# Kernel optimization log

Measured on AMD Instinct MI355X. Metric: run time of the kernel, lower is better.

## Reference

```python
import jax, jax.numpy as jnp
import numpy as np
from jax import lax

MAX_DIST_THR = 10.0
R = 10  # window radius: any distance < thr has per-axis offset <= 9, so R=10 is exact after clamping
INF = jnp.float32(1e12)


def _min_pass(c, axis):
    # 1D min-convolution with squared offsets: out[i] = min_k (c[i+k-R] + (k-R)^2)
    n = c.shape[axis]
    pad = [(0, 0)] * c.ndim
    pad[axis] = (R, R)
    p = jnp.pad(c, pad, constant_values=INF)
    out = None
    for k in range(2 * R + 1):
        v = lax.slice_in_dim(p, k, k + n, axis=axis) + jnp.float32((k - R) ** 2)
        out = v if out is None else jnp.minimum(out, v)
    return out


def _clamped_edt(fg):
    # Euclidean distance to nearest True pixel, exact where < MAX_DIST_THR, clamped above.
    cost = jnp.where(fg, jnp.float32(0.0), INF)  # [B,1,H,W]
    d2 = _min_pass(_min_pass(cost, 2), 3)
    return jnp.minimum(jnp.sqrt(d2), jnp.float32(MAX_DIST_THR))


def reference(gt, pred):
    thr = jnp.float32(MAX_DIST_THR)
    D_gt = lax.stop_gradient(_clamped_edt(gt > 0.5))
    D_est = lax.stop_gradient(_clamped_edt(pred > 0.5))
    mask_D_gt = D_gt < thr
    filt_sum = jnp.sum(pred * mask_D_gt)
    # ch[ch > thr] = thr  ==  minimum (values are non-negative)
    ch1 = jnp.minimum(D_gt * pred, thr)
    ch2 = jnp.minimum(D_est * gt, thr)
    num = jnp.sum(ch1 + ch2, axis=(1, 2, 3))  # [B]
    den = jnp.mean(jnp.sum(pred, axis=(1, 2, 3)) + jnp.sum(gt, axis=(1, 2, 3)))  # scalar
    dbe_com = num / den
    return jnp.where(filt_sum == 0, thr, dbe_com)


def setup_inputs() -> dict:
    key = jax.random.key(0)
    k1, k2 = jax.random.split(key)
    shape = (1, 1, 2048, 4096)
    gt = jax.random.bernoulli(k1, 0.05, shape).astype(jnp.float32)
    pred = jax.random.bernoulli(k2, 0.05, shape).astype(jnp.float32)
    return {"gt": gt, "pred": pred}
```

## Files before the change

kernel.cpp:

```cpp
#include <hip/hip_runtime.h>

typedef unsigned long long u64;
typedef unsigned int u32;

#define HH 2048
#define WW 4096
#define MW 66
#define MROWS (HH + 20)
#define MASK_WORDS ((size_t)MROWS * MW)
#define MASK_BYTES (MASK_WORDS * 8)
#define THR 10.0f
#define LIST_CAP (512u * 1024u)

#define PACK_BLOCKS 2048
#define COMP_BLOCKS 256
#define SCAN_BLOCKS 1024
#define GUARD_WORDS 5416

#define GM_OFF 16384
#define PM_OFF (GM_OFF + MASK_BYTES)
#define LP_OFF (PM_OFF + MASK_BYTES)
#define LG_OFF (LP_OFF + LIST_CAP * 4)

__global__ __launch_bounds__(256) void pack_masks(const float* __restrict__ gt,
                                                  const float* __restrict__ pred,
                                                  u64* __restrict__ gm,
                                                  u64* __restrict__ pm,
                                                  u32* __restrict__ cnt) {
    int gtid = blockIdx.x * 256 + threadIdx.x;
    if (gtid < 2) cnt[gtid] = 0u;
    if (gtid < 2 * GUARD_WORDS) {
        int m = gtid >= GUARD_WORDS;
        int i = gtid - m * GUARD_WORDS;
        u64* dst = m ? pm : gm;
        int row, w;
        if (i < 660)       { row = i / 66;            w = i - row * 66; }
        else if (i < 1320) { int j = i - 660; int r = j / 66;
                             row = (MROWS - 10) + r;  w = j - r * 66; }
        else               { int j = i - 1320; row = 10 + (j >> 1);
                             w = (j & 1) ? (MW - 1) : 0; }
        dst[(size_t)row * MW + w] = 0ull;
    }

    int l = threadIdx.x & 63;
    int gw = gtid >> 6;
    #pragma unroll 1
    for (int t = 0; t < 4; ++t) {
        int tile = gw * 4 + t;
        int base = tile * 256;
        u64 g0 = __ballot(gt[base +   0 + l] > 0.5f);
        u64 g1 = __ballot(gt[base +  64 + l] > 0.5f);
        u64 g2 = __ballot(gt[base + 128 + l] > 0.5f);
        u64 g3 = __ballot(gt[base + 192 + l] > 0.5f);
        u64 p0 = __ballot(pred[base +   0 + l] > 0.5f);
        u64 p1 = __ballot(pred[base +  64 + l] > 0.5f);
        u64 p2 = __ballot(pred[base + 128 + l] > 0.5f);
        u64 p3 = __ballot(pred[base + 192 + l] > 0.5f);
        if (l < 4) {
            u64 gv = (l == 0) ? g0 : (l == 1) ? g1 : (l == 2) ? g2 : g3;
            u64 pv = (l == 0) ? p0 : (l == 1) ? p1 : (l == 2) ? p2 : p3;
            int W = tile * 4 + l;
            size_t o = (size_t)((W >> 6) + 10) * MW + 1 + (W & 63);
            gm[o] = gv;
            pm[o] = pv;
        }
    }
}

__global__ __launch_bounds__(256) void compact(const u64* __restrict__ gm,
                                               const u64* __restrict__ pm,
                                               u32* __restrict__ cnt,
                                               u32* __restrict__ listP,
                                               u32* __restrict__ listG) {
    bool isPred = blockIdx.x < (COMP_BLOCKS / 2);
    const u64* msk = isPred ? pm : gm;
    u32* lst = isPred ? listP : listG;
    u32* ctr = isPred ? cnt : cnt + 1;
    int wb = (blockIdx.x & (COMP_BLOCKS / 2 - 1)) * 1024;
    int tid = threadIdx.x;

    u64 wv[4];
    u32 tp = 0;
    #pragma unroll
    for (int j = 0; j < 4; ++j) {
        int W = wb + tid + 256 * j;
        wv[j] = msk[(size_t)((W >> 6) + 10) * MW + 1 + (W & 63)];
        tp += (u32)__popcll(wv[j]);
    }
    u32 s = tp;
    #pragma unroll
    for (int o = 1; o < 64; o <<= 1) {
        u32 v = __shfl_up(s, o);
        if ((tid & 63) >= o) s += v;
    }
    u32 excl = s - tp;
    __shared__ u32 wtot[4], wbase[4], sbase;
    int wid = tid >> 6, lane = tid & 63;
    if (lane == 63) wtot[wid] = s;
    __syncthreads();
    if (tid == 0) {
        u32 bt = 0;
        for (int i = 0; i < 4; ++i) { wbase[i] = bt; bt += wtot[i]; }
        sbase = atomicAdd(ctr, bt);
    }
    __syncthreads();
    u32 ptr = sbase + wbase[wid] + excl;
    #pragma unroll
    for (int j = 0; j < 4; ++j) {
        int W = wb + tid + 256 * j;
        u32 yx = ((u32)(W >> 6) << 12) | ((u32)(W & 63) << 6);
        u64 m = wv[j];
        while (m) {
            u32 b = (u32)__ffsll((long long)m) - 1u;
            if (ptr < LIST_CAP) lst[ptr] = yx + b;
            ++ptr;
            m &= m - 1;
        }
    }
}

__device__ __forceinline__ u32 scan_d2(const u64* __restrict__ rowc, int x) {
    int b = x + 54;
    int sh = b & 63;
    int shl = 63 - sh;
    const u64* q = rowc + (b >> 6);
    u64 q0 = q[0], q1 = q[1];
    u32 win = (u32)((q0 >> sh) | ((q1 << 1) << shl)) & 0x1FFFFFu;
    u32 hi = win >> 10;
    u32 lo = win & 0x3FFu;
    u32 dr = (u32)__ffs((int)hi) - 1u;
    u32 dl = (u32)__clz((int)lo) - 21u;
    u32 mdx = dr < dl ? dr : dl;
    u32 mind2 = mdx * mdx;
    #pragma unroll
    for (int ady = 1; ady <= 9; ++ady) {
        const u64* r0 = q - (size_t)ady * MW;
        const u64* r1 = q + (size_t)ady * MW;
        u64 a0 = r0[0] | r1[0];
        u64 a1 = r0[1] | r1[1];
        u32 w = (u32)((a0 >> sh) | ((a1 << 1) << shl)) & 0x1FFFFFu;
        u32 h2 = w >> 10;
        u32 l2 = w & 0x3FFu;
        u32 d1 = (u32)__ffs((int)h2) - 1u;
        u32 d0 = (u32)__clz((int)l2) - 21u;
        u32 m2 = d1 < d0 ? d1 : d0;
        u32 d2 = (u32)(ady * ady) + m2 * m2;
        mind2 = d2 < mind2 ? d2 : mind2;
    }
    return mind2;
}

__global__ __launch_bounds__(256) void dbe_scan(const u64* __restrict__ gm,
                                                const u64* __restrict__ pm,
                                                const u32* __restrict__ cnt,
                                                const u32* __restrict__ listP,
                                                const u32* __restrict__ listG,
                                                float* __restrict__ pn,
                                                float* __restrict__ pf) {
    u32 cp = cnt[0], cg = cnt[1];
    u32 total = cp + cg;
    float num = 0.0f, filt = 0.0f;

    for (u32 i = blockIdx.x * 256 + threadIdx.x; i < total;
         i += SCAN_BLOCKS * 256) {
        bool isP = i < cp;
        u32 e = isP ? listP[i] : listG[i - cp];
        u32 x = e & 4095u;
        u32 y = e >> 12;
        const u64* base = isP ? gm : pm;
        u32 d2 = scan_d2(base + (size_t)(y + 10) * MW, (int)x);
        num += fminf(sqrtf((float)d2), THR);
        filt += (isP && d2 < 100u) ? 1.0f : 0.0f;
    }

    #pragma unroll
    for (int o = 32; o > 0; o >>= 1) {
        num += __shfl_down(num, o);
        filt += __shfl_down(filt, o);
    }
    __shared__ float sN[4], sF[4];
    int lane = threadIdx.x & 63, wid = threadIdx.x >> 6;
    if (lane == 0) { sN[wid] = num; sF[wid] = filt; }
    __syncthreads();
    if (threadIdx.x == 0) {
        pn[blockIdx.x] = sN[0] + sN[1] + sN[2] + sN[3];
        pf[blockIdx.x] = sF[0] + sF[1] + sF[2] + sF[3];
    }
}

__global__ __launch_bounds__(256) void dbe_reduce(const float* __restrict__ pn,
                                                  const float* __restrict__ pf,
                                                  const u32* __restrict__ cnt,
                                                  float* __restrict__ out) {
    double n = 0.0, f = 0.0;
    for (int i = threadIdx.x; i < SCAN_BLOCKS; i += 256) {
        n += (double)pn[i];
        f += (double)pf[i];
    }
    #pragma unroll
    for (int o = 32; o > 0; o >>= 1) {
        n += __shfl_down(n, o);
        f += __shfl_down(f, o);
    }
    __shared__ double sn[4], sf[4];
    int lane = threadIdx.x & 63, wid = threadIdx.x >> 6;
    if (lane == 0) { sn[wid] = n; sf[wid] = f; }
    __syncthreads();
    if (threadIdx.x == 0) {
        double N = sn[0] + sn[1] + sn[2] + sn[3];
        double F = sf[0] + sf[1] + sf[2] + sf[3];
        double den = (double)(cnt[0] + cnt[1]);
        out[0] = (F == 0.0) ? THR : (float)(N / den);
    }
}

extern "C" void kernel_launch(void* const* d_in, const int* in_sizes, int n_in,
                              void* d_out, int out_size, void* d_ws, size_t ws_size,
                              hipStream_t stream) {
    const float* gt   = (const float*)d_in[0];
    const float* pred = (const float*)d_in[1];
    float* out = (float*)d_out;

    char* ws = (char*)d_ws;
    u32* cnt = (u32*)ws;
    float* pn = (float*)(ws + 256);
    float* pf = (float*)(ws + 4352);
    u64* gm = (u64*)(ws + GM_OFF);
    u64* pm = (u64*)(ws + PM_OFF);
    u32* listP = (u32*)(ws + LP_OFF);
    u32* listG = (u32*)(ws + LG_OFF);

    pack_masks<<<PACK_BLOCKS, 256, 0, stream>>>(gt, pred, gm, pm, cnt);
    compact<<<COMP_BLOCKS, 256, 0, stream>>>(gm, pm, cnt, listP, listG);
    dbe_scan<<<SCAN_BLOCKS, 256, 0, stream>>>(gm, pm, cnt, listP, listG, pn, pf);
    dbe_reduce<<<1, 256, 0, stream>>>(pn, pf, cnt, out);
}
```

Measured before the change: 116.0 us.

## Fuse mask packing with compaction into per-block segmented lists

Merges the pack and compact kernels into one. Each block packs 128 words of both masks, then writes its set-pixel coordinates into a fixed-size per-block segment using local prefix sums. This removes the global atomic counter, one kernel launch and the re-read of the packed masks. The scan kernel then processes one segment per block, and the reduce kernel totals the per-block counts for the denominator. A segment has room for 2048 entries against at most 8192 bits per block, and the bounds check on list writes is gone, so dense inputs would overflow into neighbouring segments.

```diff
diff --git a/kernel.cpp b/kernel.cpp
--- a/kernel.cpp
+++ b/kernel.cpp
@@ -10,25 +10,31 @@
 #define MASK_WORDS ((size_t)MROWS * MW)
 #define MASK_BYTES (MASK_WORDS * 8)
 #define THR 10.0f
-#define LIST_CAP (512u * 1024u)
-
-#define PACK_BLOCKS 2048
-#define COMP_BLOCKS 256
-#define SCAN_BLOCKS 1024
+
+#define FUSED_BLOCKS 1024
+#define SCAN_BLOCKS  1024
+#define SEG 2048
 #define GUARD_WORDS 5416
 
 #define GM_OFF 16384
 #define PM_OFF (GM_OFF + MASK_BYTES)
 #define LP_OFF (PM_OFF + MASK_BYTES)
-#define LG_OFF (LP_OFF + LIST_CAP * 4)
-
-__global__ __launch_bounds__(256) void pack_masks(const float* __restrict__ gt,
-                                                  const float* __restrict__ pred,
-                                                  u64* __restrict__ gm,
-                                                  u64* __restrict__ pm,
-                                                  u32* __restrict__ cnt) {
-    int gtid = blockIdx.x * 256 + threadIdx.x;
-    if (gtid < 2) cnt[gtid] = 0u;
+#define LG_OFF (LP_OFF + (size_t)SEG * FUSED_BLOCKS * 4)
+
+__global__ __launch_bounds__(256) void pack_compact(const float* __restrict__ gt,
+                                                    const float* __restrict__ pred,
+                                                    u64* __restrict__ gm,
+                                                    u64* __restrict__ pm,
+                                                    u32* __restrict__ cntPb,
+                                                    u32* __restrict__ cntGb,
+                                                    u32* __restrict__ listP,
+                                                    u32* __restrict__ listG) {
+    int tid = threadIdx.x;
+    int l = tid & 63;
+    int wv = tid >> 6;
+    int b = blockIdx.x;
+
+    int gtid = b * 256 + tid;
     if (gtid < 2 * GUARD_WORDS) {
         int m = gtid >= GUARD_WORDS;
         int i = gtid - m * GUARD_WORDS;
@@ -42,80 +48,67 @@
         dst[(size_t)row * MW + w] = 0ull;
     }
 
-    int l = threadIdx.x & 63;
-    int gw = gtid >> 6;
+    int wbase = b * 128 + wv * 32;
+    int idx = (l < 32) ? l : (l - 32);
+    u64 myw = 0;
     #pragma unroll 1
-    for (int t = 0; t < 4; ++t) {
-        int tile = gw * 4 + t;
-        int base = tile * 256;
-        u64 g0 = __ballot(gt[base +   0 + l] > 0.5f);
-        u64 g1 = __ballot(gt[base +  64 + l] > 0.5f);
-        u64 g2 = __ballot(gt[base + 128 + l] > 0.5f);
-        u64 g3 = __ballot(gt[base + 192 + l] > 0.5f);
-        u64 p0 = __ballot(pred[base +   0 + l] > 0.5f);
-        u64 p1 = __ballot(pred[base +  64 + l] > 0.5f);
-        u64 p2 = __ballot(pred[base + 128 + l] > 0.5f);
-        u64 p3 = __ballot(pred[base + 192 + l] > 0.5f);
-        if (l < 4) {
-            u64 gv = (l == 0) ? g0 : (l == 1) ? g1 : (l == 2) ? g2 : g3;
-            u64 pv = (l == 0) ? p0 : (l == 1) ? p1 : (l == 2) ? p2 : p3;
-            int W = tile * 4 + l;
-            size_t o = (size_t)((W >> 6) + 10) * MW + 1 + (W & 63);
-            gm[o] = gv;
-            pm[o] = pv;
+    for (int t = 0; t < 8; ++t) {
+        int w0 = wbase + 4 * t;
+        size_t px = (size_t)w0 * 64 + l;
+        u64 g0 = __ballot(gt[px +   0] > 0.5f);
+        u64 g1 = __ballot(gt[px +  64] > 0.5f);
+        u64 g2 = __ballot(gt[px + 128] > 0.5f);
+        u64 g3 = __ballot(gt[px + 192] > 0.5f);
+        u64 p0 = __ballot(pred[px +   0] > 0.5f);
+        u64 p1 = __ballot(pred[px +  64] > 0.5f);
+        u64 p2 = __ballot(pred[px + 128] > 0.5f);
+        u64 p3 = __ballot(pred[px + 192] > 0.5f);
+        if ((idx >> 2) == t) {
+            int j = idx & 3;
+            u64 gsel = (j == 0) ? g0 : (j == 1) ? g1 : (j == 2) ? g2 : g3;
+            u64 psel = (j == 0) ? p0 : (j == 1) ? p1 : (j == 2) ? p2 : p3;
+            myw = (l < 32) ? gsel : psel;
         }
     }
-}
-
-__global__ __launch_bounds__(256) void compact(const u64* __restrict__ gm,
-                                               const u64* __restrict__ pm,
-                                               u32* __restrict__ cnt,
-                                               u32* __restrict__ listP,
-                                               u32* __restrict__ listG) {
-    bool isPred = blockIdx.x < (COMP_BLOCKS / 2);
-    const u64* msk = isPred ? pm : gm;
-    u32* lst = isPred ? listP : listG;
-    u32* ctr = isPred ? cnt : cnt + 1;
-    int wb = (blockIdx.x & (COMP_BLOCKS / 2 - 1)) * 1024;
-    int tid = threadIdx.x;
-
-    u64 wv[4];
-    u32 tp = 0;
-    #pragma unroll
-    for (int j = 0; j < 4; ++j) {
-        int W = wb + tid + 256 * j;
-        wv[j] = msk[(size_t)((W >> 6) + 10) * MW + 1 + (W & 63)];
-        tp += (u32)__popcll(wv[j]);
-    }
-    u32 s = tp;
-    #pragma unroll
-    for (int o = 1; o < 64; o <<= 1) {
-        u32 v = __shfl_up(s, o);
-        if ((tid & 63) >= o) s += v;
-    }
-    u32 excl = s - tp;
-    __shared__ u32 wtot[4], wbase[4], sbase;
-    int wid = tid >> 6, lane = tid & 63;
-    if (lane == 63) wtot[wid] = s;
+
+    int myW = wbase + idx;
+    size_t o = (size_t)((myW >> 6) + 10) * MW + 1 + (myW & 63);
+    if (l < 32) gm[o] = myw; else pm[o] = myw;
+
+    u32 pc = (u32)__popcll(myw);
+    u32 s = pc;
+    #pragma unroll
+    for (int off = 1; off < 64; off <<= 1) {
+        u32 v = __shfl_up(s, off);
+        if (l >= off) s += v;
+    }
+    u32 excl = s - pc;
+    u32 gtot = __shfl(s, 31);
+    u32 tot  = __shfl(s, 63);
+    u32 ptot = tot - gtot;
+
+    __shared__ u32 wg[4], wp[4];
+    if (l == 0) { wg[wv] = gtot; wp[wv] = ptot; }
     __syncthreads();
+    u32 gbase = 0, pbase = 0;
+    #pragma unroll
+    for (int i = 0; i < 4; ++i) {
+        gbase += (i < wv) ? wg[i] : 0u;
+        pbase += (i < wv) ? wp[i] : 0u;
+    }
     if (tid == 0) {
-        u32 bt = 0;
-        for (int i = 0; i < 4; ++i) { wbase[i] = bt; bt += wtot[i]; }
-        sbase = atomicAdd(ctr, bt);
-    }
-    __syncthreads();
-    u32 ptr = sbase + wbase[wid] + excl;
-    #pragma unroll
-    for (int j = 0; j < 4; ++j) {
-        int W = wb + tid + 256 * j;
-        u32 yx = ((u32)(W >> 6) << 12) | ((u32)(W & 63) << 6);
-        u64 m = wv[j];
-        while (m) {
-            u32 b = (u32)__ffsll((long long)m) - 1u;
-            if (ptr < LIST_CAP) lst[ptr] = yx + b;
-            ++ptr;
-            m &= m - 1;
-        }
+        cntGb[b] = wg[0] + wg[1] + wg[2] + wg[3];
+        cntPb[b] = wp[0] + wp[1] + wp[2] + wp[3];
+    }
+
+    u32 ptr = (l < 32) ? (gbase + excl) : (pbase + (excl - gtot));
+    u32* lst = ((l < 32) ? listG : listP) + (size_t)b * SEG;
+    u32 e0 = (u32)myW << 6;
+    u64 m = myw;
+    while (m) {
+        u32 bit = (u32)__ffsll((long long)m) - 1u;
+        lst[ptr++] = e0 + bit;
+        m &= m - 1;
     }
 }
 
@@ -152,19 +145,22 @@
 
 __global__ __launch_bounds__(256) void dbe_scan(const u64* __restrict__ gm,
                                                 const u64* __restrict__ pm,
-                                                const u32* __restrict__ cnt,
+                                                const u32* __restrict__ cntPb,
+                                                const u32* __restrict__ cntGb,
                                                 const u32* __restrict__ listP,
                                                 const u32* __restrict__ listG,
                                                 float* __restrict__ pn,
                                                 float* __restrict__ pf) {
-    u32 cp = cnt[0], cg = cnt[1];
+    int b = blockIdx.x;
+    u32 cp = cntPb[b], cg = cntGb[b];
     u32 total = cp + cg;
+    const u32* segP = listP + (size_t)b * SEG;
+    const u32* segG = listG + (size_t)b * SEG;
     float num = 0.0f, filt = 0.0f;
 
-    for (u32 i = blockIdx.x * 256 + threadIdx.x; i < total;
-         i += SCAN_BLOCKS * 256) {
+    for (u32 i = threadIdx.x; i < total; i += 256) {
         bool isP = i < cp;
-        u32 e = isP ? listP[i] : listG[i - cp];
+        u32 e = isP ? segP[i] : segG[i - cp];
         u32 x = e & 4095u;
         u32 y = e >> 12;
         const u64* base = isP ? gm : pm;
@@ -183,33 +179,38 @@
     if (lane == 0) { sN[wid] = num; sF[wid] = filt; }
     __syncthreads();
     if (threadIdx.x == 0) {
-        pn[blockIdx.x] = sN[0] + sN[1] + sN[2] + sN[3];
-        pf[blockIdx.x] = sF[0] + sF[1] + sF[2] + sF[3];
+        pn[b] = sN[0] + sN[1] + sN[2] + sN[3];
+        pf[b] = sF[0] + sF[1] + sF[2] + sF[3];
     }
 }
 
 __global__ __launch_bounds__(256) void dbe_reduce(const float* __restrict__ pn,
                                                   const float* __restrict__ pf,
-                                                  const u32* __restrict__ cnt,
+                                                  const u32* __restrict__ cntPb,
+                                                  const u32* __restrict__ cntGb,
                                                   float* __restrict__ out) {
     double n = 0.0, f = 0.0;
+    u32 c = 0;
     for (int i = threadIdx.x; i < SCAN_BLOCKS; i += 256) {
         n += (double)pn[i];
         f += (double)pf[i];
+        c += cntPb[i] + cntGb[i];
     }
     #pragma unroll
     for (int o = 32; o > 0; o >>= 1) {
         n += __shfl_down(n, o);
         f += __shfl_down(f, o);
+        c += __shfl_down(c, o);
     }
     __shared__ double sn[4], sf[4];
+    __shared__ u32 sc[4];
     int lane = threadIdx.x & 63, wid = threadIdx.x >> 6;
-    if (lane == 0) { sn[wid] = n; sf[wid] = f; }
+    if (lane == 0) { sn[wid] = n; sf[wid] = f; sc[wid] = c; }
     __syncthreads();
     if (threadIdx.x == 0) {
         double N = sn[0] + sn[1] + sn[2] + sn[3];
         double F = sf[0] + sf[1] + sf[2] + sf[3];
-        double den = (double)(cnt[0] + cnt[1]);
+        double den = (double)(sc[0] + sc[1] + sc[2] + sc[3]);
         out[0] = (F == 0.0) ? THR : (float)(N / den);
     }
 }
@@ -222,16 +223,18 @@
     float* out = (float*)d_out;
 
     char* ws = (char*)d_ws;
-    u32* cnt = (u32*)ws;
-    float* pn = (float*)(ws + 256);
-    float* pf = (float*)(ws + 4352);
+    u32* cntPb = (u32*)ws;
+    u32* cntGb = (u32*)(ws + 4096);
+    float* pn = (float*)(ws + 8192);
+    float* pf = (float*)(ws + 12288);
     u64* gm = (u64*)(ws + GM_OFF);
     u64* pm = (u64*)(ws + PM_OFF);
     u32* listP = (u32*)(ws + LP_OFF);
     u32* listG = (u32*)(ws + LG_OFF);
 
-    pack_masks<<<PACK_BLOCKS, 256, 0, stream>>>(gt, pred, gm, pm, cnt);
-    compact<<<COMP_BLOCKS, 256, 0, stream>>>(gm, pm, cnt, listP, listG);
-    dbe_scan<<<SCAN_BLOCKS, 256, 0, stream>>>(gm, pm, cnt, listP, listG, pn, pf);
-    dbe_reduce<<<1, 256, 0, stream>>>(pn, pf, cnt, out);
-}
+    pack_compact<<<FUSED_BLOCKS, 256, 0, stream>>>(gt, pred, gm, pm,
+                                                   cntPb, cntGb, listP, listG);
+    dbe_scan<<<SCAN_BLOCKS, 256, 0, stream>>>(gm, pm, cntPb, cntGb,
+                                              listP, listG, pn, pf);
+    dbe_reduce<<<1, 256, 0, stream>>>(pn, pf, cntPb, cntGb, out);
+}
```

After: 107.9 us. 1.07x faster.
